# Kernel tuning notes

Hardware: AMD Instinct MI355X
Metric: run time of the kernel (lower is better)

The kernel has to match this reference:

```python
import jax, jax.numpy as jnp
import numpy as np

N = 100000
E = 1600000
IN_DIM, HID, OUT = 512, 256, 32
EPS = 1e-16  # matches PyG softmax denominator epsilon


def gat_layer(xp, a_src, a_dst, src, dst, n_nodes):
    """Single-head GAT propagate with sigmoid + segment softmax, scatter-add.
    xp: [N, C] projected features; a_src/a_dst: [N] per-node attention logits;
    src/dst: [E] edge endpoints (message flows src -> dst)."""
    alpha = jax.nn.sigmoid(a_src[src] + a_dst[dst])  # [E]
    m = jax.ops.segment_max(alpha, dst, num_segments=n_nodes)  # [N]
    ex = jnp.exp(alpha - m[dst])
    denom = jax.ops.segment_sum(ex, dst, num_segments=n_nodes)  # [N]
    a = ex / (denom[dst] + EPS)  # [E]
    msg = xp[src] * a[:, None]  # [E, C]
    return jax.ops.segment_sum(msg, dst, num_segments=n_nodes)  # [N, C]


def setup_inputs() -> dict:
    key = jax.random.key(0)
    k1, k2, k3, k4, k5, k6, k7, k8 = jax.random.split(key, 8)
    features = jax.random.normal(k1, (N, IN_DIM), dtype=jnp.float32)
    edge_index = jax.random.randint(k2, (2, E), 0, N, dtype=jnp.int64)
    g = 1.414
    W1 = jax.random.normal(k3, (IN_DIM, HID), dtype=jnp.float32) * (g * np.sqrt(2.0 / (IN_DIM + HID)))
    W2 = jax.random.normal(k4, (HID, OUT), dtype=jnp.float32) * (g * np.sqrt(2.0 / (HID + OUT)))
    att_src1 = jax.random.normal(k5, (HID,), dtype=jnp.float32) * (g * np.sqrt(2.0 / (1 + HID)))
    att_dst1 = jax.random.normal(k6, (HID,), dtype=jnp.float32) * (g * np.sqrt(2.0 / (1 + HID)))
    return {"features": features, "edge_index": edge_index, "W1": W1, "W2": W2,
            "att_src1": att_src1, "att_dst1": att_dst1}


def reference(features, edge_index, W1, W2, att_src1, att_dst1):
    src, dst = edge_index[0], edge_index[1]
    # conv1 (with attention)
    xp1 = features @ W1  # [N, HID]
    a_src = xp1 @ att_src1  # [N]
    a_dst = xp1 @ att_dst1  # [N]
    h1 = jax.nn.elu(gat_layer(xp1, a_src, a_dst, src, dst, N))
    # conv2 (attention=False -> plain linear, mean over 1 head)
    h2 = h1 @ W2  # [N, OUT]
    # conv3: weights tied to W2^T, attention tied to conv1's per-node logits
    xp3 = h2 @ W2.T  # [N, HID]
    h3 = jax.nn.elu(gat_layer(xp3, a_src, a_dst, src, dst, N))
    # conv4 (attention=False): weights tied to W1^T
    h4 = h3 @ W1.T  # [N, IN_DIM]
    return h2, h4
```

## Files before the change

kernel.cpp:

```cpp
#include <hip/hip_runtime.h>
#include <cstdint>
#include <cstddef>

#define INDIM 512
#define HIDD  256
#define OUTD  32

typedef __attribute__((ext_vector_type(4))) float f32x4;
typedef __attribute__((ext_vector_type(8))) short bf16x8;

static inline __device__ float b2f(unsigned short u) {
  union { float f; unsigned int i; } v; v.i = ((unsigned int)u) << 16; return v.f;
}
static inline __device__ unsigned short f2b(float f) {
  union { float f; unsigned int i; } v; v.f = f;
  unsigned int x = v.i;
  x += 0x7fffu + ((x >> 16) & 1u);
  return (unsigned short)(x >> 16);
}

static inline __device__ float edgew(float x) {
  float al = 1.f / (1.f + __expf(-x));
  return __expf(al);
}

static __device__ __forceinline__ void gld16(const unsigned short* g, unsigned short* l) {
  __builtin_amdgcn_global_load_lds(
      (const __attribute__((address_space(1))) void*)g,
      (__attribute__((address_space(3))) void*)l, 16, 0, 0);
}

__global__ __launch_bounds__(256) void probe_kernel(
    const unsigned int* __restrict__ feat, const unsigned int* __restrict__ eidx,
    int* __restrict__ flags)
{
  int t = threadIdx.x;
  __shared__ int cnt, oddnz;
  if (t == 0) { cnt = 0; oddnz = 0; }
  __syncthreads();
  unsigned int w = feat[t];
  unsigned short lo = (unsigned short)(w & 0xFFFFu);
  int e = (lo >> 7) & 0xFF;
  int plausible = ((lo & 0x7FFF) == 0) || (e >= 0x60 && e <= 0x9F);
  atomicAdd(&cnt, plausible);
  if (t & 1) { if (eidx[t] != 0u) atomicAdd(&oddnz, 1); }
  __syncthreads();
  if (t == 0) { flags[0] = (cnt >= 192) ? 1 : 0; flags[1] = (oddnz == 0) ? 1 : 0; }
}

__global__ __launch_bounds__(256) void deg_kernel(
    const unsigned int* __restrict__ eidx, int* __restrict__ deg, int E,
    const int* __restrict__ flags)
{
  int e = blockIdx.x * 256 + threadIdx.x;
  if (e >= E) return;
  int d = flags[1] ? (int)eidx[2 * ((size_t)E + e)] : (int)eidx[(size_t)E + e];
  atomicAdd(&deg[d], 1);
}

static inline __device__ float ldadapt(const void* p, size_t i, int isbf) {
  return isbf ? b2f(((const unsigned short*)p)[i]) : ((const float*)p)[i];
}

__global__ __launch_bounds__(256) void convb_kernel(
    const void* __restrict__ in, unsigned short* __restrict__ outb, size_t n4,
    const int* __restrict__ flags)
{
  const int fb = flags[0];
  size_t i = (size_t)blockIdx.x * 256 + threadIdx.x;
  size_t stride = (size_t)gridDim.x * 256;
  if (fb) {
    const ushort4* ip = (const ushort4*)in;
    ushort4* op = (ushort4*)outb;
    for (; i < n4; i += stride) op[i] = ip[i];
  } else {
    const float4* ip = (const float4*)in;
    ushort4* op = (ushort4*)outb;
    for (; i < n4; i += stride) {
      float4 v = ip[i];
      ushort4 o; o.x = f2b(v.x); o.y = f2b(v.y); o.z = f2b(v.z); o.w = f2b(v.w);
      op[i] = o;
    }
  }
}

__global__ __launch_bounds__(256) void prep_weights(
    const void* __restrict__ W1, const void* __restrict__ W2,
    const void* __restrict__ aS, const void* __restrict__ aD,
    unsigned short* __restrict__ W1b, unsigned short* __restrict__ W1tb,
    float* __restrict__ W2f, unsigned short* __restrict__ W2b64,
    float* __restrict__ atS, float* __restrict__ atD,
    const int* __restrict__ flags)
{
  const int fb = flags[0];
  int i = blockIdx.x * 256 + threadIdx.x;
  if (i < INDIM * HIDD) {
    int r = i >> 8, c = i & 255;
    float w0 = ldadapt(W1, i, fb);
    unsigned short wb = f2b(w0);
    W1b[i] = wb;
    W1tb[c * INDIM + r] = wb;
  }
  if (i < HIDD * OUTD) {
    int r = i >> 5, c = i & 31;
    float w0 = ldadapt(W2, i, fb);
    W2f[i] = w0;
    W2b64[r * 64 + c] = f2b(w0);
    W2b64[r * 64 + 32 + c] = 0;
  }
  if (i < HIDD) { atS[i] = ldadapt(aS, i, fb); atD[i] = ldadapt(aD, i, fb); }
}

template<int OUTMODE, int EPI>
__global__ __launch_bounds__(256) void gemm_nt2(
    const unsigned short* __restrict__ A, const unsigned short* __restrict__ Bt,
    unsigned short* __restrict__ Cb, void* __restrict__ Out, size_t outOff,
    const int* __restrict__ flags, int M, int Nn, int K)
{
  __shared__ unsigned short Als[128 * 64];
  __shared__ unsigned short Bls[128 * 64];
  const int tid = threadIdx.x, lane = tid & 63, wid = tid >> 6;
  const int wr = wid >> 1, wc = wid & 1;
  const int rowBase = blockIdx.y * 128, colBase = blockIdx.x * 128;
  const int fb = flags[0];

  const int srow = (lane >> 3), sg = lane & 7;

  f32x4 acc[4][4] = {};

  for (int kt = 0; kt < K; kt += 64) {
#pragma unroll
    for (int i = 0; i < 4; ++i) {
      int row = wid * 32 + i * 8 + srow;
      gld16(A + (size_t)(rowBase + row) * K + kt + sg * 8, Als + (wid * 4 + i) * 512);
      gld16(Bt + (size_t)(colBase + row) * K + kt + sg * 8, Bls + (wid * 4 + i) * 512);
    }
    __syncthreads();

    bf16x8 af[4], bfr[4];
#pragma unroll
    for (int ks = 0; ks < 2; ++ks) {
      int g = ks * 4 + (lane >> 4);
#pragma unroll
      for (int mi = 0; mi < 4; ++mi) {
        int row = wr * 64 + mi * 16 + (lane & 15);
        af[mi] = *(const bf16x8*)(Als + row * 64 + g * 8);
      }
#pragma unroll
      for (int ni = 0; ni < 4; ++ni) {
        int row = wc * 64 + ni * 16 + (lane & 15);
        bfr[ni] = *(const bf16x8*)(Bls + row * 64 + g * 8);
      }
#pragma unroll
      for (int mi = 0; mi < 4; ++mi)
#pragma unroll
        for (int ni = 0; ni < 4; ++ni)
          acc[mi][ni] = __builtin_amdgcn_mfma_f32_16x16x32_bf16(af[mi], bfr[ni], acc[mi][ni], 0, 0, 0);
    }
    __syncthreads();
  }

#pragma unroll
  for (int mi = 0; mi < 4; ++mi) {
    int r0 = rowBase + wr * 64 + mi * 16 + (lane >> 4) * 4;
#pragma unroll
    for (int ni = 0; ni < 4; ++ni) {
      int c = colBase + wc * 64 + ni * 16 + (lane & 15);
#pragma unroll
      for (int v = 0; v < 4; ++v) {
        int r = r0 + v;
        if (r < M) {
          size_t idx = (size_t)r * Nn + c;
          float x = acc[mi][ni][v];
          if (EPI) x = x > 0.f ? x : expm1f(x);
          if (OUTMODE == 0) Cb[idx] = f2b(x);
          else {
            if (fb) ((unsigned short*)Out)[outOff + idx] = f2b(x);
            else    ((float*)Out)[outOff + idx] = x;
          }
        }
      }
    }
  }
}

__global__ __launch_bounds__(256) void rowdots(
    const unsigned short* __restrict__ P, const float* __restrict__ atS,
    const float* __restrict__ atD,
    float* __restrict__ asrc, float* __restrict__ adst, int N)
{
  int wave = threadIdx.x >> 6, lane = threadIdx.x & 63;
  int node = blockIdx.x * 4 + wave;
  if (node >= N) return;
  ushort4 u = *(const ushort4*)(P + (size_t)node * HIDD + lane * 4);
  float4 v = make_float4(b2f(u.x), b2f(u.y), b2f(u.z), b2f(u.w));
  float4 s = *(const float4*)(atS + lane * 4);
  float4 d = *(const float4*)(atD + lane * 4);
  float s1 = v.x * s.x + v.y * s.y + v.z * s.z + v.w * s.w;
  float s2 = v.x * d.x + v.y * d.y + v.z * d.z + v.w * d.w;
#pragma unroll
  for (int off = 32; off; off >>= 1) {
    s1 += __shfl_down(s1, off);
    s2 += __shfl_down(s2, off);
  }
  if (lane == 0) { asrc[node] = s1; adst[node] = s2; }
}

__global__ __launch_bounds__(256) void scan_p1(const int* __restrict__ deg,
                                               int* __restrict__ bsum, int N)
{
  int b = blockIdx.x, t = threadIdx.x;
  int i0 = b * 1024 + t * 4;
  int s = 0;
#pragma unroll
  for (int j = 0; j < 4; ++j) { int i = i0 + j; if (i < N) s += deg[i]; }
  __shared__ int red[256];
  red[t] = s;
  __syncthreads();
  for (int o = 128; o; o >>= 1) {
    if (t < o) red[t] += red[t + o];
    __syncthreads();
  }
  if (t == 0) bsum[b] = red[0];
}

__global__ __launch_bounds__(256) void scan_p2(int* __restrict__ bsum, int nb)
{
  __shared__ int sh[256];
  int t = threadIdx.x;
  int v = (t < nb) ? bsum[t] : 0;
  sh[t] = v;
  __syncthreads();
  for (int o = 1; o < 256; o <<= 1) {
    int u = (t >= o) ? sh[t - o] : 0;
    __syncthreads();
    sh[t] += u;
    __syncthreads();
  }
  if (t < nb) bsum[t] = sh[t] - v;
}

__global__ __launch_bounds__(256) void scan_p3(const int* __restrict__ deg,
                                               const int* __restrict__ bsum,
                                               int* __restrict__ offs, int* __restrict__ cur,
                                               int N, int nb)
{
  int b = blockIdx.x, t = threadIdx.x;
  int i0 = b * 1024 + t * 4;
  int v[4]; int s = 0;
#pragma unroll
  for (int j = 0; j < 4; ++j) { int i = i0 + j; v[j] = (i < N) ? deg[i] : 0; s += v[j]; }
  __shared__ int sh[256];
  sh[t] = s;
  __syncthreads();
  for (int o = 1; o < 256; o <<= 1) {
    int u = (t >= o) ? sh[t - o] : 0;
    __syncthreads();
    sh[t] += u;
    __syncthreads();
  }
  int run = bsum[b] + sh[t] - s;
#pragma unroll
  for (int j = 0; j < 4; ++j) {
    int i = i0 + j;
    if (i < N) { offs[i] = run; cur[i] = run; }
    run += v[j];
  }
  if (b == nb - 1 && t == 255) offs[N] = run;
}

__global__ __launch_bounds__(256) void fill_kernel(
    const unsigned int* __restrict__ eidx, int* __restrict__ cur,
    int* __restrict__ srcP, int E, const int* __restrict__ flags)
{
  int e = blockIdx.x * 256 + threadIdx.x;
  if (e >= E) return;
  int s, d;
  if (flags[1]) {
    s = (int)eidx[2 * (size_t)e];
    d = (int)eidx[2 * ((size_t)E + e)];
  } else {
    s = (int)eidx[e];
    d = (int)eidx[(size_t)E + e];
  }
  int pos = atomicAdd(&cur[d], 1);
  srcP[pos] = s;
}

__global__ __launch_bounds__(256) void agg_elu2(
    const unsigned short* __restrict__ xp,
    const float* __restrict__ asrc, const float* __restrict__ adst,
    const int* __restrict__ srcP, const int* __restrict__ offs,
    unsigned short* __restrict__ hout, int N)
{
  __shared__ int   sS[4][64];
  __shared__ float sW[4][64];
  int wid = threadIdx.x >> 6, lane = threadIdx.x & 63;
  int node = blockIdx.x * 4 + wid;
  if (node >= N) return;
  const float ad = adst[node];
  int s0 = offs[node], s1 = offs[node + 1];
  float a0 = 0.f, a1 = 0.f, a2 = 0.f, a3 = 0.f, den = 0.f;
  for (int base = s0; base < s1; base += 64) {
    int cnt = s1 - base; if (cnt > 64) cnt = 64;
    if (lane < cnt) {
      int sv = srcP[base + lane];
      sS[wid][lane] = sv;
      sW[wid][lane] = edgew(asrc[sv] + ad);
    }
    asm volatile("s_waitcnt lgkmcnt(0)" ::: "memory");
    int j = 0;
    for (; j + 8 <= cnt; j += 8) {
      ushort4 u[8];
#pragma unroll
      for (int q = 0; q < 8; ++q)
        u[q] = *(const ushort4*)(xp + (size_t)sS[wid][j + q] * HIDD + lane * 4);
#pragma unroll
      for (int q = 0; q < 8; ++q) {
        float wv = sW[wid][j + q];
        den += wv;
        a0 += wv * b2f(u[q].x); a1 += wv * b2f(u[q].y);
        a2 += wv * b2f(u[q].z); a3 += wv * b2f(u[q].w);
      }
    }
    for (; j < cnt; ++j) {
      int   sv = sS[wid][j];
      float wv = sW[wid][j];
      den += wv;
      ushort4 u = *(const ushort4*)(xp + (size_t)sv * HIDD + lane * 4);
      a0 += wv * b2f(u.x); a1 += wv * b2f(u.y); a2 += wv * b2f(u.z); a3 += wv * b2f(u.w);
    }
  }
  float inv = 1.f / (den + 1e-16f);
  float r0 = a0 * inv, r1 = a1 * inv, r2 = a2 * inv, r3 = a3 * inv;
  r0 = r0 > 0.f ? r0 : expm1f(r0);
  r1 = r1 > 0.f ? r1 : expm1f(r1);
  r2 = r2 > 0.f ? r2 : expm1f(r2);
  r3 = r3 > 0.f ? r3 : expm1f(r3);
  ushort4 o; o.x = f2b(r0); o.y = f2b(r1); o.z = f2b(r2); o.w = f2b(r3);
  *(ushort4*)(hout + (size_t)node * HIDD + lane * 4) = o;
}

__global__ __launch_bounds__(256) void gemm_h2(
    const unsigned short* __restrict__ H1, const float* __restrict__ W2f,
    void* __restrict__ Out, unsigned short* __restrict__ h2b,
    const int* __restrict__ flags, int M)
{
  const int fb = flags[0];
  __shared__ float Bs[HIDD][33];
  __shared__ float As[8][HIDD];
  int tid = threadIdx.x;
  int tx = tid & 31, ty = tid >> 5;
  int row0 = blockIdx.x * 8;
#pragma unroll
  for (int j = 0; j < 32; ++j) {
    int idx = tid + 256 * j;
    Bs[idx >> 5][idx & 31] = W2f[idx];
  }
#pragma unroll
  for (int j = 0; j < 8; ++j) {
    int idx = tid + 256 * j;
    int r = idx >> 8, k = idx & 255;
    As[r][k] = (row0 + r < M) ? b2f(H1[(size_t)(row0 + r) * HIDD + k]) : 0.f;
  }
  __syncthreads();
  float acc = 0.f;
#pragma unroll 8
  for (int k = 0; k < HIDD; ++k) acc += As[ty][k] * Bs[k][tx];
  int row = row0 + ty;
  if (row < M) {
    size_t idx = (size_t)row * OUTD + tx;
    if (fb) ((unsigned short*)Out)[idx] = f2b(acc);
    else    ((float*)Out)[idx] = acc;
    h2b[idx] = f2b(acc);
  }
}

__global__ __launch_bounds__(256) void agg_small(
    const unsigned short* __restrict__ h2b,
    const float* __restrict__ asrc, const float* __restrict__ adst,
    const int* __restrict__ srcP, const int* __restrict__ offs,
    unsigned short* __restrict__ g2pad, int N)
{
  int wid = threadIdx.x >> 6, lane = threadIdx.x & 63;
  int node = blockIdx.x * 4 + wid;
  if (node >= N) return;
  int grp = lane >> 4, cl = lane & 15;
  const float ad = adst[node];
  int s0 = offs[node], s1 = offs[node + 1];
  float a0 = 0.f, a1 = 0.f, den = 0.f;
  for (int e = s0 + grp; e < s1; e += 4) {
    int   sv = srcP[e];
    float wv = edgew(asrc[sv] + ad);
    den += wv;
    ushort2 u = *(const ushort2*)(h2b + (size_t)sv * OUTD + cl * 2);
    a0 += wv * b2f(u.x);
    a1 += wv * b2f(u.y);
  }
  a0 += __shfl_xor(a0, 16); a0 += __shfl_xor(a0, 32);
  a1 += __shfl_xor(a1, 16); a1 += __shfl_xor(a1, 32);
  den += __shfl_xor(den, 16); den += __shfl_xor(den, 32);
  if (grp == 0) {
    float inv = 1.f / (den + 1e-16f);
    ushort2 o; o.x = f2b(a0 * inv); o.y = f2b(a1 * inv);
    *(ushort2*)(g2pad + (size_t)node * 64 + cl * 2) = o;
  } else if (grp == 1) {
    *(ushort2*)(g2pad + (size_t)node * 64 + 32 + cl * 2) = make_ushort2(0, 0);
  }
}

extern "C" void kernel_launch(void* const* d_in, const int* in_sizes, int n_in,
                              void* d_out, int out_size, void* d_ws, size_t ws_size,
                              hipStream_t stream)
{
  const void*         feat = d_in[0];
  const unsigned int* eidx = (const unsigned int*)d_in[1];
  const void*         W1   = d_in[2];
  const void*         W2   = d_in[3];
  const void*         aS   = d_in[4];
  const void*         aD   = d_in[5];

  const int N = in_sizes[0] / INDIM;
  const int E = in_sizes[1] / 2;
  const int M_pad = ((N + 127) / 128) * 128;
  const int nb = (N + 1023) / 1024;

  char* w = (char*)d_ws;
  auto alloc = [&](size_t bytes) -> char* {
    char* p = w; w += (bytes + 255) & ~(size_t)255; return p;
  };
  unsigned short* featb = (unsigned short*)alloc((size_t)M_pad * INDIM * 2);
  unsigned short* H     = featb;
  unsigned short* P     = (unsigned short*)alloc((size_t)M_pad * HIDD * 2);
  unsigned short* h2b   = (unsigned short*)alloc((size_t)N * OUTD * 2);
  unsigned short* g2pad = (unsigned short*)alloc((size_t)M_pad * 64 * 2);
  float* asrc = (float*)alloc((size_t)N * 4);
  float* adst = (float*)alloc((size_t)N * 4);
  int*   srcP = (int*)alloc((size_t)E * 4);
  int*   deg  = (int*)alloc((size_t)N * 4);
  int*   offs = (int*)alloc((size_t)(N + 1) * 4);
  int*   cur  = (int*)alloc((size_t)N * 4);
  int*   bsum = (int*)alloc((size_t)(nb + 1) * 4);
  unsigned short* W1b   = (unsigned short*)alloc((size_t)INDIM * HIDD * 2);
  unsigned short* W1tb  = (unsigned short*)alloc((size_t)INDIM * HIDD * 2);
  unsigned short* W2b64 = (unsigned short*)alloc((size_t)HIDD * 64 * 2);
  float* W2f  = (float*)alloc((size_t)HIDD * OUTD * 4);
  float* atS  = (float*)alloc((size_t)HIDD * 4);
  float* atD  = (float*)alloc((size_t)HIDD * 4);
  int*   flags = (int*)alloc(64);

  hipMemsetAsync(deg, 0, (size_t)N * 4, stream);

  probe_kernel<<<1, 256, 0, stream>>>((const unsigned int*)feat, eidx, flags);

  const int eb = (E + 255) / 256;
  deg_kernel<<<eb, 256, 0, stream>>>(eidx, deg, E, flags);
  prep_weights<<<512, 256, 0, stream>>>(W1, W2, aS, aD, W1b, W1tb, W2f, W2b64, atS, atD, flags);

  convb_kernel<<<2048, 256, 0, stream>>>(feat, featb, (size_t)N * INDIM / 4, flags);

  const int mb = (N + 127) / 128;

  gemm_nt2<0, 0><<<dim3(HIDD / 128, mb), 256, 0, stream>>>(
      featb, W1tb, P, nullptr, 0, flags, N, HIDD, INDIM);

  rowdots<<<(N + 3) / 4, 256, 0, stream>>>(P, atS, atD, asrc, adst, N);

  scan_p1<<<nb, 256, 0, stream>>>(deg, bsum, N);
  scan_p2<<<1, 256, 0, stream>>>(bsum, nb);
  scan_p3<<<nb, 256, 0, stream>>>(deg, bsum, offs, cur, N, nb);

  fill_kernel<<<eb, 256, 0, stream>>>(eidx, cur, srcP, E, flags);

  agg_elu2<<<(N + 3) / 4, 256, 0, stream>>>(P, asrc, adst, srcP, offs, H, N);

  gemm_h2<<<(N + 7) / 8, 256, 0, stream>>>(H, W2f, d_out, h2b, flags, N);

  agg_small<<<(N + 3) / 4, 256, 0, stream>>>(h2b, asrc, adst, srcP, offs, g2pad, N);

  gemm_nt2<0, 1><<<dim3(HIDD / 128, mb), 256, 0, stream>>>(
      g2pad, W2b64, H, nullptr, 0, flags, N, HIDD, 64);

  gemm_nt2<1, 0><<<dim3(INDIM / 128, mb), 256, 0, stream>>>(
      H, W1b, nullptr, d_out, (size_t)N * OUTD, flags, N, INDIM, HIDD);
}
```

Baseline: 730.2 us.

## Fuse feature bf16 conversion into first GEMM and partition edges by destination slab

Result: slower. 818.1 us (+12.0%).

```diff
diff --git a/kernel.cpp b/kernel.cpp
--- a/kernel.cpp
+++ b/kernel.cpp
@@ -5,6 +5,7 @@
 #define INDIM 512
 #define HIDD  256
 #define OUTD  32
+#define PCH   4096
 
 typedef __attribute__((ext_vector_type(4))) float f32x4;
 typedef __attribute__((ext_vector_type(8))) short bf16x8;
@@ -48,40 +49,93 @@
   if (t == 0) { flags[0] = (cnt >= 192) ? 1 : 0; flags[1] = (oddnz == 0) ? 1 : 0; }
 }
 
-__global__ __launch_bounds__(256) void deg_kernel(
-    const unsigned int* __restrict__ eidx, int* __restrict__ deg, int E,
+__global__ __launch_bounds__(256) void p1_kernel(
+    const unsigned int* __restrict__ eidx, int* __restrict__ deg,
+    int* __restrict__ slabCount, int E, int shift, int nslab,
     const int* __restrict__ flags)
 {
-  int e = blockIdx.x * 256 + threadIdx.x;
-  if (e >= E) return;
-  int d = flags[1] ? (int)eidx[2 * ((size_t)E + e)] : (int)eidx[(size_t)E + e];
-  atomicAdd(&deg[d], 1);
+  __shared__ int hist[64];
+  int t = threadIdx.x;
+  if (t < 64) hist[t] = 0;
+  __syncthreads();
+  int e = blockIdx.x * 256 + t;
+  if (e < E) {
+    int d = flags[1] ? (int)eidx[2 * ((size_t)E + e)] : (int)eidx[(size_t)E + e];
+    atomicAdd(&deg[d], 1);
+    atomicAdd(&hist[d >> shift], 1);
+  }
+  __syncthreads();
+  if (t < nslab && hist[t]) atomicAdd(&slabCount[t], hist[t]);
+}
+
+__global__ __launch_bounds__(64) void slabscan_kernel(
+    const int* __restrict__ slabCount, int* __restrict__ slabOff,
+    int* __restrict__ slabCur, int nslab)
+{
+  int t = threadIdx.x;
+  int v = (t < nslab) ? slabCount[t] : 0;
+  int inc = v;
+#pragma unroll
+  for (int o = 1; o < 64; o <<= 1) {
+    int u = __shfl_up(inc, o);
+    if (t >= o) inc += u;
+  }
+  int exc = inc - v;
+  if (t < nslab) { slabOff[t] = exc; slabCur[t] = exc; }
+  if (t == 63) slabOff[nslab] = inc;
+}
+
+__global__ __launch_bounds__(256) void part_kernel(
+    const unsigned int* __restrict__ eidx, int* __restrict__ slabCur,
+    uint2* __restrict__ part, int E, int shift, int nslab,
+    const int* __restrict__ flags)
+{
+  __shared__ int hist[64], base[64];
+  int t = threadIdx.x;
+  int e0 = blockIdx.x * PCH;
+  const int i64 = flags[1];
+  if (t < 64) hist[t] = 0;
+  __syncthreads();
+  for (int i = t; i < PCH; i += 256) {
+    int e = e0 + i; if (e >= E) break;
+    int d = i64 ? (int)eidx[2 * ((size_t)E + e)] : (int)eidx[(size_t)E + e];
+    atomicAdd(&hist[d >> shift], 1);
+  }
+  __syncthreads();
+  if (t < nslab) {
+    base[t] = hist[t] ? atomicAdd(&slabCur[t], hist[t]) : 0;
+    hist[t] = 0;
+  }
+  __syncthreads();
+  for (int i = t; i < PCH; i += 256) {
+    int e = e0 + i; if (e >= E) break;
+    int s, d;
+    if (i64) { s = (int)eidx[2 * (size_t)e]; d = (int)eidx[2 * ((size_t)E + e)]; }
+    else     { s = (int)eidx[e];             d = (int)eidx[(size_t)E + e]; }
+    int sl = d >> shift;
+    int r = atomicAdd(&hist[sl], 1);
+    part[(size_t)base[sl] + r] = make_uint2((unsigned)s, (unsigned)d);
+  }
+}
+
+__global__ __launch_bounds__(256) void fill2_kernel(
+    const uint2* __restrict__ part, const int* __restrict__ slabOff,
+    int* __restrict__ cur, int* __restrict__ srcP, int nslab)
+{
+  int xcd = blockIdx.x & 7, j = blockIdx.x >> 3;
+  int t = threadIdx.x;
+  for (int sl = xcd; sl < nslab; sl += 8) {
+    int s0 = slabOff[sl], s1 = slabOff[sl + 1];
+    for (int i = s0 + j * 256 + t; i < s1; i += 64 * 256) {
+      uint2 p = part[i];
+      int pos = atomicAdd(&cur[p.y], 1);
+      srcP[pos] = (int)p.x;
+    }
+  }
 }
 
 static inline __device__ float ldadapt(const void* p, size_t i, int isbf) {
   return isbf ? b2f(((const unsigned short*)p)[i]) : ((const float*)p)[i];
-}
-
-__global__ __launch_bounds__(256) void convb_kernel(
-    const void* __restrict__ in, unsigned short* __restrict__ outb, size_t n4,
-    const int* __restrict__ flags)
-{
-  const int fb = flags[0];
-  size_t i = (size_t)blockIdx.x * 256 + threadIdx.x;
-  size_t stride = (size_t)gridDim.x * 256;
-  if (fb) {
-    const ushort4* ip = (const ushort4*)in;
-    ushort4* op = (ushort4*)outb;
-    for (; i < n4; i += stride) op[i] = ip[i];
-  } else {
-    const float4* ip = (const float4*)in;
-    ushort4* op = (ushort4*)outb;
-    for (; i < n4; i += stride) {
-      float4 v = ip[i];
-      ushort4 o; o.x = f2b(v.x); o.y = f2b(v.y); o.z = f2b(v.z); o.w = f2b(v.w);
-      op[i] = o;
-    }
-  }
 }
 
 __global__ __launch_bounds__(256) void prep_weights(
@@ -111,9 +165,9 @@
   if (i < HIDD) { atS[i] = ldadapt(aS, i, fb); atD[i] = ldadapt(aD, i, fb); }
 }
 
-template<int OUTMODE, int EPI>
+template<int AMODE, int OUTMODE, int EPI>
 __global__ __launch_bounds__(256) void gemm_nt2(
-    const unsigned short* __restrict__ A, const unsigned short* __restrict__ Bt,
+    const void* __restrict__ Av, const unsigned short* __restrict__ Bt,
     unsigned short* __restrict__ Cb, void* __restrict__ Out, size_t outOff,
     const int* __restrict__ flags, int M, int Nn, int K)
 {
@@ -129,10 +183,33 @@
   f32x4 acc[4][4] = {};
 
   for (int kt = 0; kt < K; kt += 64) {
+    if (AMODE == 1 && !fb) {
+      const float* Af = (const float*)Av;
+#pragma unroll
+      for (int i = 0; i < 4; ++i) {
+        int row = wid * 32 + i * 8 + srow;
+        int gr = rowBase + row; if (gr > M - 1) gr = M - 1;
+        const float* sp = Af + (size_t)gr * K + kt + sg * 8;
+        float4 lo = *(const float4*)sp;
+        float4 hi = *(const float4*)(sp + 4);
+        union { unsigned short us[8]; int4 v; } cv;
+        cv.us[0] = f2b(lo.x); cv.us[1] = f2b(lo.y); cv.us[2] = f2b(lo.z); cv.us[3] = f2b(lo.w);
+        cv.us[4] = f2b(hi.x); cv.us[5] = f2b(hi.y); cv.us[6] = f2b(hi.z); cv.us[7] = f2b(hi.w);
+        *(int4*)(Als + (wid * 4 + i) * 512 + lane * 8) = cv.v;
+      }
+    } else {
+      const unsigned short* Ab = (const unsigned short*)Av;
+#pragma unroll
+      for (int i = 0; i < 4; ++i) {
+        int row = wid * 32 + i * 8 + srow;
+        int gr = rowBase + row;
+        if (AMODE == 1 && gr > M - 1) gr = M - 1;
+        gld16(Ab + (size_t)gr * K + kt + sg * 8, Als + (wid * 4 + i) * 512);
+      }
+    }
 #pragma unroll
     for (int i = 0; i < 4; ++i) {
       int row = wid * 32 + i * 8 + srow;
-      gld16(A + (size_t)(rowBase + row) * K + kt + sg * 8, Als + (wid * 4 + i) * 512);
       gld16(Bt + (size_t)(colBase + row) * K + kt + sg * 8, Bls + (wid * 4 + i) * 512);
     }
     __syncthreads();
@@ -267,24 +344,6 @@
     run += v[j];
   }
   if (b == nb - 1 && t == 255) offs[N] = run;
-}
-
-__global__ __launch_bounds__(256) void fill_kernel(
-    const unsigned int* __restrict__ eidx, int* __restrict__ cur,
-    int* __restrict__ srcP, int E, const int* __restrict__ flags)
-{
-  int e = blockIdx.x * 256 + threadIdx.x;
-  if (e >= E) return;
-  int s, d;
-  if (flags[1]) {
-    s = (int)eidx[2 * (size_t)e];
-    d = (int)eidx[2 * ((size_t)E + e)];
-  } else {
-    s = (int)eidx[e];
-    d = (int)eidx[(size_t)E + e];
-  }
-  int pos = atomicAdd(&cur[d], 1);
-  srcP[pos] = s;
 }
 
 __global__ __launch_bounds__(256) void agg_elu2(
@@ -424,23 +483,29 @@
   const int E = in_sizes[1] / 2;
   const int M_pad = ((N + 127) / 128) * 128;
   const int nb = (N + 1023) / 1024;
+  int shift = 11;
+  while ((((N - 1) >> shift) + 1) > 64) ++shift;
+  const int nslab = ((N - 1) >> shift) + 1;
 
   char* w = (char*)d_ws;
   auto alloc = [&](size_t bytes) -> char* {
     char* p = w; w += (bytes + 255) & ~(size_t)255; return p;
   };
-  unsigned short* featb = (unsigned short*)alloc((size_t)M_pad * INDIM * 2);
-  unsigned short* H     = featb;
+  unsigned short* H     = (unsigned short*)alloc((size_t)M_pad * HIDD * 2);
   unsigned short* P     = (unsigned short*)alloc((size_t)M_pad * HIDD * 2);
   unsigned short* h2b   = (unsigned short*)alloc((size_t)N * OUTD * 2);
   unsigned short* g2pad = (unsigned short*)alloc((size_t)M_pad * 64 * 2);
   float* asrc = (float*)alloc((size_t)N * 4);
   float* adst = (float*)alloc((size_t)N * 4);
   int*   srcP = (int*)alloc((size_t)E * 4);
+  uint2* part = (uint2*)alloc((size_t)E * 8);
   int*   deg  = (int*)alloc((size_t)N * 4);
   int*   offs = (int*)alloc((size_t)(N + 1) * 4);
   int*   cur  = (int*)alloc((size_t)N * 4);
   int*   bsum = (int*)alloc((size_t)(nb + 1) * 4);
+  int*   slabCount = (int*)alloc(64 * 4);
+  int*   slabOff   = (int*)alloc(65 * 4);
+  int*   slabCur   = (int*)alloc(64 * 4);
   unsigned short* W1b   = (unsigned short*)alloc((size_t)INDIM * HIDD * 2);
   unsigned short* W1tb  = (unsigned short*)alloc((size_t)INDIM * HIDD * 2);
   unsigned short* W2b64 = (unsigned short*)alloc((size_t)HIDD * 64 * 2);
@@ -450,27 +515,26 @@
   int*   flags = (int*)alloc(64);
 
   hipMemsetAsync(deg, 0, (size_t)N * 4, stream);
+  hipMemsetAsync(slabCount, 0, 64 * 4, stream);
 
   probe_kernel<<<1, 256, 0, stream>>>((const unsigned int*)feat, eidx, flags);
 
   const int eb = (E + 255) / 256;
-  deg_kernel<<<eb, 256, 0, stream>>>(eidx, deg, E, flags);
+  p1_kernel<<<eb, 256, 0, stream>>>(eidx, deg, slabCount, E, shift, nslab, flags);
+  slabscan_kernel<<<1, 64, 0, stream>>>(slabCount, slabOff, slabCur, nslab);
+  part_kernel<<<(E + PCH - 1) / PCH, 256, 0, stream>>>(eidx, slabCur, part, E, shift, nslab, flags);
   prep_weights<<<512, 256, 0, stream>>>(W1, W2, aS, aD, W1b, W1tb, W2f, W2b64, atS, atD, flags);
-
-  convb_kernel<<<2048, 256, 0, stream>>>(feat, featb, (size_t)N * INDIM / 4, flags);
-
-  const int mb = (N + 127) / 128;
-
-  gemm_nt2<0, 0><<<dim3(HIDD / 128, mb), 256, 0, stream>>>(
-      featb, W1tb, P, nullptr, 0, flags, N, HIDD, INDIM);
-
-  rowdots<<<(N + 3) / 4, 256, 0, stream>>>(P, atS, atD, asrc, adst, N);
-
   scan_p1<<<nb, 256, 0, stream>>>(deg, bsum, N);
   scan_p2<<<1, 256, 0, stream>>>(bsum, nb);
   scan_p3<<<nb, 256, 0, stream>>>(deg, bsum, offs, cur, N, nb);
-
-  fill_kernel<<<eb, 256, 0, stream>>>(eidx, cur, srcP, E, flags);
+  fill2_kernel<<<512, 256, 0, stream>>>(part, slabOff, cur, srcP, nslab);
+
+  const int mb = (N + 127) / 128;
+
+  gemm_nt2<1, 0, 0><<<dim3(HIDD / 128, mb), 256, 0, stream>>>(
+      feat, W1tb, P, nullptr, 0, flags, N, HIDD, INDIM);
+
+  rowdots<<<(N + 3) / 4, 256, 0, stream>>>(P, atS, atD, asrc, adst, N);
 
   agg_elu2<<<(N + 3) / 4, 256, 0, stream>>>(P, asrc, adst, srcP, offs, H, N);
 
@@ -478,9 +542,9 @@
 
   agg_small<<<(N + 3) / 4, 256, 0, stream>>>(h2b, asrc, adst, srcP, offs, g2pad, N);
 
-  gemm_nt2<0, 1><<<dim3(HIDD / 128, mb), 256, 0, stream>>>(
+  gemm_nt2<0, 0, 1><<<dim3(HIDD / 128, mb), 256, 0, stream>>>(
       g2pad, W2b64, H, nullptr, 0, flags, N, HIDD, 64);
 
-  gemm_nt2<1, 0><<<dim3(INDIM / 128, mb), 256, 0, stream>>>(
+  gemm_nt2<0, 1, 0><<<dim3(INDIM / 128, mb), 256, 0, stream>>>(
       H, W1b, nullptr, d_out, (size_t)N * OUTD, flags, N, INDIM, HIDD);
 }
```
